# Optimization experiments

Hardware: AMD Instinct MI355X
Metric: run time of the kernel (lower is better)

Reference implementation:

```python
import jax, jax.numpy as jnp
import numpy as np

B, N, D = 4, 2048, 512
H, HD = 8, 64  # heads, output_dim per head


def setup_inputs() -> dict:
    key = jax.random.key(0)
    ks = jax.random.split(key, 6)
    x = jax.random.normal(ks[0], (B, N, D), dtype=jnp.float32)
    adj = (jax.random.uniform(ks[1], (N, N)) < 0.1).astype(jnp.float32)
    adj = jnp.maximum(adj, jnp.eye(N, dtype=jnp.float32))
    s = 0.02
    Wq = jax.random.normal(ks[2], (D, H * HD), dtype=jnp.float32) * s
    Wk = jax.random.normal(ks[3], (D, H * HD), dtype=jnp.float32) * s
    Wv = jax.random.normal(ks[4], (D, H * HD), dtype=jnp.float32) * s
    bq = jnp.zeros((H * HD,), dtype=jnp.float32)
    bk = jnp.zeros((H * HD,), dtype=jnp.float32)
    bv = jnp.zeros((H * HD,), dtype=jnp.float32)
    return {"x": x, "adj": adj, "Wq": Wq, "bq": bq, "Wk": Wk, "bk": bk, "Wv": Wv, "bv": bv}


def reference(x, adj, Wq, bq, Wk, bk, Wv, bv):
    b, n, _ = x.shape
    q = (x @ Wq + bq).reshape(b, n, H, HD)
    k = (x @ Wk + bk).reshape(b, n, H, HD)
    v = (x @ Wv + bv).reshape(b, n, H, HD)
    # scores: [b, h, i, j]
    scores = jnp.einsum('bihd,bjhd->bhij', q, k) / jnp.sqrt(jnp.float32(HD))
    mask = jnp.where(adj == 0, jnp.float32(-1e9), jnp.float32(0.0))  # [n, n]
    scores = scores + mask[None, None, :, :]
    weights = jax.nn.softmax(scores, axis=-1)
    # dropout is identity at inference (training=False)
    out = jnp.einsum('bhij,bjhd->bihd', weights, v)
    return out.reshape(b, n, H * HD)
```

## Files before the change

kernel.cpp:

```cpp
#include <hip/hip_runtime.h>
#include <hip/hip_bf16.h>
#include <stdint.h>

#define NTOK 2048
#define DIN  512
#define QSCALE 0.18033688011112042f

typedef __attribute__((ext_vector_type(8))) short bf16x8;
typedef __attribute__((ext_vector_type(4))) short bf16x4;
typedef __attribute__((ext_vector_type(4))) float f32x4;

#define MFMA16(a, b, c) __builtin_amdgcn_mfma_f32_16x16x32_bf16((a), (b), (c), 0, 0, 0)

static __device__ __forceinline__ short f2bf(float f) {
  union { float f; uint32_t u; } v; v.f = f;
  uint32_t r = (v.u + 0x7FFFu + ((v.u >> 16) & 1u)) >> 16;
  return (short)r;
}

__global__ __launch_bounds__(256) void k_xbf(const float* __restrict__ x, short* __restrict__ xb) {
  size_t i = (size_t)blockIdx.x * 256 + threadIdx.x;
  const float4 v = *(const float4*)(x + i * 4);
  bf16x4 h;
  h[0] = f2bf(v.x); h[1] = f2bf(v.y); h[2] = f2bf(v.z); h[3] = f2bf(v.w);
  *(bf16x4*)(xb + i * 4) = h;
}

__global__ __launch_bounds__(256) void k_wt(const float* __restrict__ W, short* __restrict__ Wt) {
  __shared__ float tile[32][33];
  int bo = blockIdx.x * 32, bc = blockIdx.y * 32;
  int tx = threadIdx.x & 31, ty = threadIdx.x >> 5;
#pragma unroll
  for (int q = 0; q < 4; ++q)
    tile[ty + q * 8][tx] = W[(bc + ty + q * 8) * DIN + bo + tx];
  __syncthreads();
#pragma unroll
  for (int q = 0; q < 4; ++q)
    Wt[(bo + ty + q * 8) * DIN + bc + tx] = f2bf(tile[tx][ty + q * 8]);
}

__global__ __launch_bounds__(256) void k_mask(const float* __restrict__ adj,
                                              unsigned long long* __restrict__ m64) {
  int wid = ((blockIdx.x * blockDim.x + threadIdx.x) >> 6);
  int lane = threadIdx.x & 63;
  int i = wid >> 5, wd = wid & 31;
  float a = adj[i * NTOK + wd * 64 + lane];
  unsigned long long b = __ballot(a != 0.0f);
  if (lane == 0) m64[i * 32 + wd] = b;
}

__global__ __launch_bounds__(256) void k_qkv(const short* __restrict__ xb,
                                             const short* __restrict__ Wt,
                                             const float* __restrict__ bq,
                                             const float* __restrict__ bk,
                                             const float* __restrict__ bv,
                                             short* __restrict__ Qb, short* __restrict__ Kb,
                                             short* __restrict__ Vb) {
  __shared__ short As[128 * 40];
  __shared__ short Bs[128 * 40];
  const int z = blockIdx.z;
  const short* Wz = Wt + z * DIN * DIN;
  const float* bias = (z == 0) ? bq : ((z == 1) ? bk : bv);
  const int mbase = blockIdx.x * 128, nbase = blockIdx.y * 128;
  const int tid = threadIdx.x;
  const int lane = tid & 63, w = tid >> 6;
  const int wr = w >> 1, wc = w & 1;
  const int lrow = lane & 15, lgrp = lane >> 4;

  f32x4 acc[4][4];
#pragma unroll
  for (int a = 0; a < 4; ++a)
#pragma unroll
    for (int b = 0; b < 4; ++b) acc[a][b] = (f32x4){0.f, 0.f, 0.f, 0.f};

  for (int kb = 0; kb < DIN; kb += 32) {
#pragma unroll
    for (int t = 0; t < 2; ++t) {
      int idx = tid + t * 256;
      int r = idx >> 2, c8 = idx & 3;
      *(bf16x8*)(As + r * 40 + c8 * 8) =
          *(const bf16x8*)(xb + (size_t)(mbase + r) * DIN + kb + c8 * 8);
    }
#pragma unroll
    for (int t = 0; t < 2; ++t) {
      int idx = tid + t * 256;
      int r = idx >> 2, c8 = idx & 3;
      *(bf16x8*)(Bs + r * 40 + c8 * 8) =
          *(const bf16x8*)(Wz + (size_t)(nbase + r) * DIN + kb + c8 * 8);
    }
    __syncthreads();
    bf16x8 af[4], bf[4];
#pragma unroll
    for (int mi = 0; mi < 4; ++mi)
      af[mi] = *(bf16x8*)(As + (wr * 64 + mi * 16 + lrow) * 40 + lgrp * 8);
#pragma unroll
    for (int ni = 0; ni < 4; ++ni)
      bf[ni] = *(bf16x8*)(Bs + (wc * 64 + ni * 16 + lrow) * 40 + lgrp * 8);
#pragma unroll
    for (int mi = 0; mi < 4; ++mi)
#pragma unroll
      for (int ni = 0; ni < 4; ++ni) acc[mi][ni] = MFMA16(af[mi], bf[ni], acc[mi][ni]);
    __syncthreads();
  }

#pragma unroll
  for (int ni = 0; ni < 4; ++ni) {
    int go = nbase + wc * 64 + ni * 16 + lrow;
    float bv_ = bias[go];
    int h = go >> 6, d = go & 63;
#pragma unroll
    for (int mi = 0; mi < 4; ++mi) {
#pragma unroll
      for (int v = 0; v < 4; ++v) {
        int gm = mbase + wr * 64 + mi * 16 + lgrp * 4 + v;
        int b = gm >> 11, n = gm & 2047;
        int bh = b * 8 + h;
        float val = acc[mi][ni][v] + bv_;
        if (z == 0)
          Qb[(size_t)bh * (NTOK * 64) + n * 64 + d] = f2bf(val * QSCALE);
        else if (z == 1)
          Kb[(size_t)bh * (NTOK * 64) + n * 64 + d] = f2bf(val);
        else
          Vb[(size_t)bh * (64 * NTOK) + d * NTOK + n] = f2bf(val);
      }
    }
  }
}

__global__ __launch_bounds__(256, 5) void k_attn(const short* __restrict__ Qb,
                                                 const short* __restrict__ Kb,
                                                 const short* __restrict__ Vb,
                                                 const unsigned long long* __restrict__ m64,
                                                 float* __restrict__ out) {
  __shared__ short Kl[64 * 72];
  __shared__ short Vl[64 * 72];
  __shared__ short Pl[4][16 * 72];
  const int itile = blockIdx.x, bh = blockIdx.y;
  const int ibase = itile * 64;
  const int tid = threadIdx.x, lane = tid & 63, w = tid >> 6;
  const int lrow = lane & 15, lgrp = lane >> 4;

  const short* Qp = Qb + (size_t)bh * (NTOK * 64);
  const short* Kp = Kb + (size_t)bh * (NTOK * 64);
  const short* Vp = Vb + (size_t)bh * (64 * NTOK);

  const int qrow = ibase + w * 16 + lrow;
  bf16x8 qa[2];
  qa[0] = *(const bf16x8*)(Qp + (size_t)qrow * 64 + lgrp * 8);
  qa[1] = *(const bf16x8*)(Qp + (size_t)qrow * 64 + 32 + lgrp * 8);

  const unsigned long long* mword = m64 + (size_t)qrow * 32;

  const int r0 = tid >> 3, s0 = tid & 7;

  f32x4 oacc[4];
#pragma unroll
  for (int dn = 0; dn < 4; ++dn) oacc[dn] = (f32x4){0.f, 0.f, 0.f, 0.f};
  float lrun = 0.f;

  uint4 pfK0 = *(const uint4*)(Kp + (size_t)r0 * 64 + s0 * 8);
  uint4 pfK1 = *(const uint4*)(Kp + (size_t)(r0 + 32) * 64 + s0 * 8);
  uint4 pfV0 = *(const uint4*)(Vp + (size_t)r0 * NTOK + s0 * 8);
  uint4 pfV1 = *(const uint4*)(Vp + (size_t)(r0 + 32) * NTOK + s0 * 8);
  unsigned long long mw = mword[0];
  *(uint4*)(Kl + r0 * 72 + s0 * 8) = pfK0;
  *(uint4*)(Kl + (r0 + 32) * 72 + s0 * 8) = pfK1;
  *(uint4*)(Vl + r0 * 72 + s0 * 8) = pfV0;
  *(uint4*)(Vl + (r0 + 32) * 72 + s0 * 8) = pfV1;
  __syncthreads();

  for (int jt = 0; jt < 32; ++jt) {
    unsigned long long mw_nxt = 0;
    if (jt < 31) {
      const int jn = (jt + 1) * 64;
      pfK0 = *(const uint4*)(Kp + (size_t)(jn + r0) * 64 + s0 * 8);
      pfK1 = *(const uint4*)(Kp + (size_t)(jn + r0 + 32) * 64 + s0 * 8);
      pfV0 = *(const uint4*)(Vp + (size_t)r0 * NTOK + jn + s0 * 8);
      pfV1 = *(const uint4*)(Vp + (size_t)(r0 + 32) * NTOK + jn + s0 * 8);
      mw_nxt = mword[jt + 1];
    }

    f32x4 sf[4];
#pragma unroll
    for (int jn = 0; jn < 4; ++jn) {
      f32x4 zz = (f32x4){0.f, 0.f, 0.f, 0.f};
      zz = MFMA16(*(bf16x8*)(Kl + (jn * 16 + lrow) * 72 + lgrp * 8), qa[0], zz);
      zz = MFMA16(*(bf16x8*)(Kl + (jn * 16 + lrow) * 72 + 32 + lgrp * 8), qa[1], zz);
      sf[jn] = zz;
    }

    uint32_t lo = ((uint32_t)mw) >> (lgrp * 4);
    uint32_t hi = ((uint32_t)(mw >> 32)) >> (lgrp * 4);
    float p[4][4];
    float ls = 0.f;
#pragma unroll
    for (int jn = 0; jn < 4; ++jn) {
      uint32_t bits = (jn < 2) ? lo : hi;
      const int sh = (jn & 1) * 16;
#pragma unroll
      for (int r = 0; r < 4; ++r) {
        float e = exp2f(sf[jn][r]);
        p[jn][r] = ((bits >> (sh + r)) & 1u) ? e : 0.f;
        ls += p[jn][r];
      }
    }
    lrun += ls;

#pragma unroll
    for (int jn = 0; jn < 4; ++jn) {
      uint32_t w0, w1;
      asm("v_cvt_pk_bf16_f32 %0, %1, %2" : "=v"(w0) : "v"(p[jn][0]), "v"(p[jn][1]));
      asm("v_cvt_pk_bf16_f32 %0, %1, %2" : "=v"(w1) : "v"(p[jn][2]), "v"(p[jn][3]));
      uint2 pk;
      pk.x = w0;
      pk.y = w1;
      *(uint2*)(Pl[w] + lrow * 72 + jn * 16 + lgrp * 4) = pk;
    }

#pragma unroll
    for (int dn = 0; dn < 4; ++dn) {
#pragma unroll
      for (int ks = 0; ks < 2; ++ks) {
        oacc[dn] = MFMA16(*(bf16x8*)(Pl[w] + lrow * 72 + ks * 32 + lgrp * 8),
                          *(bf16x8*)(Vl + (dn * 16 + lrow) * 72 + ks * 32 + lgrp * 8),
                          oacc[dn]);
      }
    }

    if (jt < 31) {
      __syncthreads();
      *(uint4*)(Kl + r0 * 72 + s0 * 8) = pfK0;
      *(uint4*)(Kl + (r0 + 32) * 72 + s0 * 8) = pfK1;
      *(uint4*)(Vl + r0 * 72 + s0 * 8) = pfV0;
      *(uint4*)(Vl + (r0 + 32) * 72 + s0 * 8) = pfV1;
      mw = mw_nxt;
      __syncthreads();
    }
  }

  float lfull = lrun;
  lfull += __shfl_xor(lfull, 16);
  lfull += __shfl_xor(lfull, 32);

  const int b = bh >> 3, h = bh & 7;
#pragma unroll
  for (int v = 0; v < 4; ++v) {
    float li = __shfl(lfull, lgrp * 4 + v);
    float inv = 1.0f / li;
    int i = ibase + w * 16 + lgrp * 4 + v;
#pragma unroll
    for (int dn = 0; dn < 4; ++dn)
      out[(size_t)(b * NTOK + i) * DIN + h * 64 + dn * 16 + lrow] = oacc[dn][v] * inv;
  }
}

extern "C" void kernel_launch(void* const* d_in, const int* in_sizes, int n_in,
                              void* d_out, int out_size, void* d_ws, size_t ws_size,
                              hipStream_t stream) {
  const float* x   = (const float*)d_in[0];
  const float* adj = (const float*)d_in[1];
  const float* Wq  = (const float*)d_in[2];
  const float* bq  = (const float*)d_in[3];
  const float* Wk  = (const float*)d_in[4];
  const float* bk  = (const float*)d_in[5];
  const float* Wv  = (const float*)d_in[6];
  const float* bv  = (const float*)d_in[7];
  float* out = (float*)d_out;

  char* ws = (char*)d_ws;
  short* Qb = (short*)(ws);
  short* Kb = (short*)(ws + (8u << 20));
  short* Vb = (short*)(ws + (16u << 20));
  short* Wt = (short*)(ws + (24u << 20));
  unsigned long long* m64 = (unsigned long long*)(ws + (26u << 20));
  short* xb = (short*)d_out;

  k_xbf<<<4096, 256, 0, stream>>>(x, xb);
  k_wt<<<dim3(16, 16), 256, 0, stream>>>(Wq, Wt);
  k_wt<<<dim3(16, 16), 256, 0, stream>>>(Wk, Wt + 262144);
  k_wt<<<dim3(16, 16), 256, 0, stream>>>(Wv, Wt + 524288);
  k_mask<<<16384, 256, 0, stream>>>(adj, m64);
  k_qkv<<<dim3(64, 4, 3), 256, 0, stream>>>(xb, Wt, bq, bk, bv, Qb, Kb, Vb);
  k_attn<<<dim3(32, 32), 256, 0, stream>>>(Qb, Kb, Vb, m64, out);
}
```

Baseline: 126.3 us.

## Process two query row groups per attention block to reuse K/V tiles

Each attention workgroup now handles 128 query rows instead of 64, with every wave computing two 16-row groups against the same K and V tiles held in shared memory. This halves global K/V loads and LDS staging per query and lets each K/V fragment read feed two MFMAs. The grid shrinks to 512 blocks, register and LDS use per block rise, and the occupancy hint drops from 5 to 3, so latency hiding may suffer.

```diff
diff --git a/kernel.cpp b/kernel.cpp
--- a/kernel.cpp
+++ b/kernel.cpp
@@ -127,16 +127,16 @@
   }
 }
 
-__global__ __launch_bounds__(256, 5) void k_attn(const short* __restrict__ Qb,
+__global__ __launch_bounds__(256, 3) void k_attn(const short* __restrict__ Qb,
                                                  const short* __restrict__ Kb,
                                                  const short* __restrict__ Vb,
                                                  const unsigned long long* __restrict__ m64,
                                                  float* __restrict__ out) {
   __shared__ short Kl[64 * 72];
   __shared__ short Vl[64 * 72];
-  __shared__ short Pl[4][16 * 72];
+  __shared__ short Pl[4][32 * 72];
   const int itile = blockIdx.x, bh = blockIdx.y;
-  const int ibase = itile * 64;
+  const int ibase = itile * 128;
   const int tid = threadIdx.x, lane = tid & 63, w = tid >> 6;
   const int lrow = lane & 15, lgrp = lane >> 4;
 
@@ -144,25 +144,30 @@
   const short* Kp = Kb + (size_t)bh * (NTOK * 64);
   const short* Vp = Vb + (size_t)bh * (64 * NTOK);
 
-  const int qrow = ibase + w * 16 + lrow;
-  bf16x8 qa[2];
-  qa[0] = *(const bf16x8*)(Qp + (size_t)qrow * 64 + lgrp * 8);
-  qa[1] = *(const bf16x8*)(Qp + (size_t)qrow * 64 + 32 + lgrp * 8);
-
-  const unsigned long long* mword = m64 + (size_t)qrow * 32;
+  bf16x8 qa[2][2];
+  const unsigned long long* mword[2];
+#pragma unroll
+  for (int ig = 0; ig < 2; ++ig) {
+    const int qrow = ibase + ig * 64 + w * 16 + lrow;
+    qa[ig][0] = *(const bf16x8*)(Qp + (size_t)qrow * 64 + lgrp * 8);
+    qa[ig][1] = *(const bf16x8*)(Qp + (size_t)qrow * 64 + 32 + lgrp * 8);
+    mword[ig] = m64 + (size_t)qrow * 32;
+  }
 
   const int r0 = tid >> 3, s0 = tid & 7;
 
-  f32x4 oacc[4];
-#pragma unroll
-  for (int dn = 0; dn < 4; ++dn) oacc[dn] = (f32x4){0.f, 0.f, 0.f, 0.f};
-  float lrun = 0.f;
+  f32x4 oacc[2][4];
+#pragma unroll
+  for (int ig = 0; ig < 2; ++ig)
+#pragma unroll
+    for (int dn = 0; dn < 4; ++dn) oacc[ig][dn] = (f32x4){0.f, 0.f, 0.f, 0.f};
+  float lrun[2] = {0.f, 0.f};
 
   uint4 pfK0 = *(const uint4*)(Kp + (size_t)r0 * 64 + s0 * 8);
   uint4 pfK1 = *(const uint4*)(Kp + (size_t)(r0 + 32) * 64 + s0 * 8);
   uint4 pfV0 = *(const uint4*)(Vp + (size_t)r0 * NTOK + s0 * 8);
   uint4 pfV1 = *(const uint4*)(Vp + (size_t)(r0 + 32) * NTOK + s0 * 8);
-  unsigned long long mw = mword[0];
+  unsigned long long mw[2] = {mword[0][0], mword[1][0]};
   *(uint4*)(Kl + r0 * 72 + s0 * 8) = pfK0;
   *(uint4*)(Kl + (r0 + 32) * 72 + s0 * 8) = pfK1;
   *(uint4*)(Vl + r0 * 72 + s0 * 8) = pfV0;
@@ -170,60 +175,56 @@
   __syncthreads();
 
   for (int jt = 0; jt < 32; ++jt) {
-    unsigned long long mw_nxt = 0;
+    unsigned long long mwn[2] = {0ull, 0ull};
     if (jt < 31) {
       const int jn = (jt + 1) * 64;
       pfK0 = *(const uint4*)(Kp + (size_t)(jn + r0) * 64 + s0 * 8);
       pfK1 = *(const uint4*)(Kp + (size_t)(jn + r0 + 32) * 64 + s0 * 8);
       pfV0 = *(const uint4*)(Vp + (size_t)r0 * NTOK + jn + s0 * 8);
       pfV1 = *(const uint4*)(Vp + (size_t)(r0 + 32) * NTOK + jn + s0 * 8);
-      mw_nxt = mword[jt + 1];
-    }
-
-    f32x4 sf[4];
+      mwn[0] = mword[0][jt + 1];
+      mwn[1] = mword[1][jt + 1];
+    }
+
 #pragma unroll
     for (int jn = 0; jn < 4; ++jn) {
-      f32x4 zz = (f32x4){0.f, 0.f, 0.f, 0.f};
-      zz = MFMA16(*(bf16x8*)(Kl + (jn * 16 + lrow) * 72 + lgrp * 8), qa[0], zz);
-      zz = MFMA16(*(bf16x8*)(Kl + (jn * 16 + lrow) * 72 + 32 + lgrp * 8), qa[1], zz);
-      sf[jn] = zz;
-    }
-
-    uint32_t lo = ((uint32_t)mw) >> (lgrp * 4);
-    uint32_t hi = ((uint32_t)(mw >> 32)) >> (lgrp * 4);
-    float p[4][4];
-    float ls = 0.f;
-#pragma unroll
-    for (int jn = 0; jn < 4; ++jn) {
-      uint32_t bits = (jn < 2) ? lo : hi;
-      const int sh = (jn & 1) * 16;
-#pragma unroll
-      for (int r = 0; r < 4; ++r) {
-        float e = exp2f(sf[jn][r]);
-        p[jn][r] = ((bits >> (sh + r)) & 1u) ? e : 0.f;
-        ls += p[jn][r];
+      const int krow = (jn * 16 + lrow) * 72;
+      bf16x8 kf0 = *(bf16x8*)(Kl + krow + lgrp * 8);
+      bf16x8 kf1 = *(bf16x8*)(Kl + krow + 32 + lgrp * 8);
+#pragma unroll
+      for (int ig = 0; ig < 2; ++ig) {
+        f32x4 zz = (f32x4){0.f, 0.f, 0.f, 0.f};
+        zz = MFMA16(kf0, qa[ig][0], zz);
+        zz = MFMA16(kf1, qa[ig][1], zz);
+        const uint32_t bits = (uint32_t)(mw[ig] >> (jn * 16 + lgrp * 4));
+        float p0 = (bits & 1u) ? exp2f(zz[0]) : 0.f;
+        float p1 = (bits & 2u) ? exp2f(zz[1]) : 0.f;
+        float p2 = (bits & 4u) ? exp2f(zz[2]) : 0.f;
+        float p3 = (bits & 8u) ? exp2f(zz[3]) : 0.f;
+        lrun[ig] += (p0 + p1) + (p2 + p3);
+        uint32_t w0, w1;
+        asm("v_cvt_pk_bf16_f32 %0, %1, %2" : "=v"(w0) : "v"(p0), "v"(p1));
+        asm("v_cvt_pk_bf16_f32 %0, %1, %2" : "=v"(w1) : "v"(p2), "v"(p3));
+        uint2 pkv;
+        pkv.x = w0;
+        pkv.y = w1;
+        *(uint2*)(Pl[w] + (ig * 16 + lrow) * 72 + jn * 16 + lgrp * 4) = pkv;
       }
     }
-    lrun += ls;
-
-#pragma unroll
-    for (int jn = 0; jn < 4; ++jn) {
-      uint32_t w0, w1;
-      asm("v_cvt_pk_bf16_f32 %0, %1, %2" : "=v"(w0) : "v"(p[jn][0]), "v"(p[jn][1]));
-      asm("v_cvt_pk_bf16_f32 %0, %1, %2" : "=v"(w1) : "v"(p[jn][2]), "v"(p[jn][3]));
-      uint2 pk;
-      pk.x = w0;
-      pk.y = w1;
-      *(uint2*)(Pl[w] + lrow * 72 + jn * 16 + lgrp * 4) = pk;
-    }
-
+
+    bf16x8 pa[2][2];
+#pragma unroll
+    for (int ig = 0; ig < 2; ++ig)
+#pragma unroll
+      for (int ks = 0; ks < 2; ++ks)
+        pa[ig][ks] = *(bf16x8*)(Pl[w] + (ig * 16 + lrow) * 72 + ks * 32 + lgrp * 8);
 #pragma unroll
     for (int dn = 0; dn < 4; ++dn) {
 #pragma unroll
       for (int ks = 0; ks < 2; ++ks) {
-        oacc[dn] = MFMA16(*(bf16x8*)(Pl[w] + lrow * 72 + ks * 32 + lgrp * 8),
-                          *(bf16x8*)(Vl + (dn * 16 + lrow) * 72 + ks * 32 + lgrp * 8),
-                          oacc[dn]);
+        bf16x8 vb = *(bf16x8*)(Vl + (dn * 16 + lrow) * 72 + ks * 32 + lgrp * 8);
+#pragma unroll
+        for (int ig = 0; ig < 2; ++ig) oacc[ig][dn] = MFMA16(pa[ig][ks], vb, oacc[ig][dn]);
       }
     }
 
@@ -233,24 +234,27 @@
       *(uint4*)(Kl + (r0 + 32) * 72 + s0 * 8) = pfK1;
       *(uint4*)(Vl + r0 * 72 + s0 * 8) = pfV0;
       *(uint4*)(Vl + (r0 + 32) * 72 + s0 * 8) = pfV1;
-      mw = mw_nxt;
+      mw[0] = mwn[0];
+      mw[1] = mwn[1];
       __syncthreads();
     }
   }
 
-  float lfull = lrun;
-  lfull += __shfl_xor(lfull, 16);
-  lfull += __shfl_xor(lfull, 32);
-
   const int b = bh >> 3, h = bh & 7;
 #pragma unroll
-  for (int v = 0; v < 4; ++v) {
-    float li = __shfl(lfull, lgrp * 4 + v);
-    float inv = 1.0f / li;
-    int i = ibase + w * 16 + lgrp * 4 + v;
-#pragma unroll
-    for (int dn = 0; dn < 4; ++dn)
-      out[(size_t)(b * NTOK + i) * DIN + h * 64 + dn * 16 + lrow] = oacc[dn][v] * inv;
+  for (int ig = 0; ig < 2; ++ig) {
+    float lfull = lrun[ig];
+    lfull += __shfl_xor(lfull, 16);
+    lfull += __shfl_xor(lfull, 32);
+#pragma unroll
+    for (int v = 0; v < 4; ++v) {
+      float li = __shfl(lfull, lgrp * 4 + v);
+      float inv = 1.0f / li;
+      int i = ibase + ig * 64 + w * 16 + lgrp * 4 + v;
+#pragma unroll
+      for (int dn = 0; dn < 4; ++dn)
+        out[(size_t)(b * NTOK + i) * DIN + h * 64 + dn * 16 + lrow] = oacc[ig][dn][v] * inv;
+    }
   }
 }
 
@@ -281,5 +285,5 @@
   k_wt<<<dim3(16, 16), 256, 0, stream>>>(Wv, Wt + 524288);
   k_mask<<<16384, 256, 0, stream>>>(adj, m64);
   k_qkv<<<dim3(64, 4, 3), 256, 0, stream>>>(xb, Wt, bq, bk, bv, Qb, Kb, Vb);
-  k_attn<<<dim3(32, 32), 256, 0, stream>>>(Qb, Kb, Vb, m64, out);
-}
+  k_attn<<<dim3(16, 32), 256, 0, stream>>>(Qb, Kb, Vb, m64, out);
+}
```

Measured after the change: 134.4 us. 1.06x slower.
